# Kernel optimization log

Hardware: AMD Instinct MI355X
Metric: run time of the kernel (lower is better)

## Reference

```python
import jax, jax.numpy as jnp
import numpy as np
from jax import lax

B, T, S, J, D = 8, 512, 32, 64, 400
R, MDU, TAGS = 256, 100, 7


def _lstm(x, Wih, Whh, bih, bhh):
    """PyTorch-convention LSTM over x [N,L,Din]; gate order i,f,g,o.
    Returns (hs, cs) each [N,L,R] in scan order (not re-flipped)."""
    N = x.shape[0]
    Rh = Whh.shape[1]
    h0 = jnp.zeros((N, Rh), x.dtype)
    xW = x @ Wih.T + (bih + bhh)  # precompute input projection [N,L,4R]

    def step(carry, xt):
        h, c = carry
        g = xt + h @ Whh.T
        i, f, gg, o = jnp.split(g, 4, axis=-1)
        c = jax.nn.sigmoid(f) * c + jax.nn.sigmoid(i) * jnp.tanh(gg)
        h = jax.nn.sigmoid(o) * jnp.tanh(c)
        return (h, c), (h, c)

    _, (hs, cs) = lax.scan(step, (h0, h0), xW.transpose(1, 0, 2))
    return hs.transpose(1, 0, 2), cs.transpose(1, 0, 2)


def setup_inputs() -> dict:
    key = jax.random.key(0)
    ks = jax.random.split(key, 40)

    def rn(i, shape, s=0.1):
        return s * jax.random.normal(ks[i], shape, jnp.float32)

    inp = {
        'input_text': rn(0, (B, T, D), 1.0),
        'input_syn': rn(1, (B, S, J, D), 1.0),
        'label': jax.random.randint(ks[2], (B, T), 0, TAGS),
        'len_context': jnp.full((B,), T, jnp.int32),
        'len_synopsis': jnp.full((B, S), J, jnp.int32),
    }
    # 6 LSTM parameter sets: context f1/b1 (in=D), synopsis f/b (in=D), modeling f/b (in=4R)
    idx = 3
    for name, din in [('f1', D), ('b1', D), ('sf', D), ('sb', D), ('mf', 4 * R), ('mb', 4 * R)]:
        inp['Wih_' + name] = rn(idx, (4 * R, din)); idx += 1
        inp['Whh_' + name] = rn(idx, (4 * R, R)); idx += 1
        inp['bih_' + name] = rn(idx, (4 * R,)); idx += 1
        inp['bhh_' + name] = rn(idx, (4 * R,)); idx += 1
    inp['W_cWh'] = rn(idx, (MDU, 2 * R)); idx += 1
    inp['W_cWu'] = rn(idx, (MDU, 2 * R)); idx += 1
    inp['W_v'] = rn(idx, (1, MDU)); idx += 1
    inp['W_sWh'] = rn(idx, (2 * R, 2 * R)); idx += 1
    inp['W_sWu'] = rn(idx, (2 * R, 2 * R)); idx += 1
    inp['W_Ws'] = rn(idx, (MDU, 2 * R)); idx += 1
    inp['W_out'] = rn(idx, (TAGS, 6 * R)); idx += 1
    inp['b_out'] = rn(idx, (TAGS,)); idx += 1
    return inp


def reference(input_text, input_syn, label, len_context, len_synopsis,
              Wih_f1, Whh_f1, bih_f1, bhh_f1,
              Wih_b1, Whh_b1, bih_b1, bhh_b1,
              Wih_sf, Whh_sf, bih_sf, bhh_sf,
              Wih_sb, Whh_sb, bih_sb, bhh_sb,
              Wih_mf, Whh_mf, bih_mf, bhh_mf,
              Wih_mb, Whh_mb, bih_mb, bhh_mb,
              W_cWh, W_cWu, W_v, W_sWh, W_sWu, W_Ws, W_out, b_out):
    B_, T_, D_ = input_text.shape
    S_, J_ = input_syn.shape[1], input_syn.shape[2]

    mask = (jnp.arange(T_)[None, :] < len_context[:, None]).astype(input_text.dtype)

    # --- representation layer: manual bi-LSTMCell; backward hiddens kept in scan order ---
    hs_f, cs_f = _lstm(input_text, Wih_f1, Whh_f1, bih_f1, bhh_f1)
    hs_b, cs_b = _lstm(input_text[:, ::-1], Wih_b1, Whh_b1, bih_b1, bhh_b1)
    H = jnp.concatenate([hs_f, hs_b], -1) * mask[..., None]   # [B,T,2R]
    m = jnp.concatenate([cs_f, cs_b], -1) * mask[..., None]   # [B,T,2R]
    x_init = jnp.zeros((B_, 1, 2 * R), input_text.dtype)
    H_full = jnp.concatenate([x_init, H], 1)                  # H_ : [B,T+1,2R]

    # --- synopsis encoder: bi-LSTM final hidden per synopsis sentence ---
    syn = input_syn.reshape(B_ * S_, J_, D_)
    sh_f, _ = _lstm(syn, Wih_sf, Whh_sf, bih_sf, bhh_sf)
    sh_b, _ = _lstm(syn[:, ::-1], Wih_sb, Whh_sb, bih_sb, bhh_sb)
    U = jnp.concatenate([sh_f[:, -1], sh_b[:, -1]], -1).reshape(B_, S_, 2 * R)

    # --- 'ff' co-attention ---
    cWh = H @ W_cWh.T                                          # [B,T,MDU]
    cWu = U @ W_cWu.T                                          # [B,S,MDU]
    z = jnp.tanh(cWh[:, :, None, :] + cWu[:, None, :, :]) @ W_v[0]  # [B,T,S]
    alpha = jax.nn.softmax(z, axis=-1)
    c = jnp.einsum('bts,bsd->btd', alpha, U)                   # [B,T,2R]

    # --- sentinel (ATT_SYN) ---
    Hprev = H_full[:, :T_]                                     # shifted: x_init, H[0..T-2]
    e = jax.nn.sigmoid(Hprev @ W_sWh.T + Hprev @ W_sWu.T)
    s = e * jnp.tanh(m)                                        # [B,T,2R]
    z_hat = jnp.tanh(s @ W_Ws.T + cWh) @ W_v[0]                # [B,T]
    alpha_hat = jax.nn.softmax(jnp.concatenate([z, z_hat[..., None]], -1), axis=-1)
    beta = alpha_hat[:, :, S_:S_ + 1]                          # [B,T,1]
    c_hat = beta * s + (1.0 - beta) * c
    G = jnp.concatenate([H, c_hat], -1)                        # [B,T,4R]

    # --- modeling bi-LSTM (standard aligned outputs) + output projection ---
    mh_f, _ = _lstm(G, Wih_mf, Whh_mf, bih_mf, bhh_mf)
    mh_b, _ = _lstm(G[:, ::-1], Wih_mb, Whh_mb, bih_mb, bhh_mb)
    M = jnp.concatenate([mh_f, mh_b[:, ::-1]], -1)             # [B,T,2R]

    logit = jnp.concatenate([G, M], -1) @ W_out.T + b_out      # [B,T,TAGS]
    return logit
```

## Files before the change

### kernel.cpp

```cpp
#include <hip/hip_runtime.h>
#include <math.h>
#include <stddef.h>


#define BB 8
#define TT 512
#define SS 32
#define JJ 64
#define DD 400
#define RR 256
#define G4 1024
#define H2 512
#define MDU_ 100
#define TAGS_ 7
#define BT (BB*TT)
#define NSEQ (BB*SS)
#define SCH 64
#define MB1 (1024*1024)

typedef __attribute__((ext_vector_type(8))) short short8;
typedef __attribute__((ext_vector_type(4))) float floatx4;
typedef __attribute__((ext_vector_type(4))) unsigned int u32x4;
typedef unsigned short u16;
typedef unsigned int u32;

struct Ptr6 { const void* p[6]; };

__device__ __forceinline__ float us2f(u16 u) {
    unsigned int v = ((unsigned int)u) << 16;
    return __builtin_bit_cast(float, v);
}
__device__ __forceinline__ u16 f2us(float f) {
    unsigned int v = __builtin_bit_cast(unsigned int, f);
    v += 0x7FFFu + ((v >> 16) & 1u);
    return (u16)(v >> 16);
}
__device__ __forceinline__ float ldin(const void* p, long i, int bf) {
    return bf ? us2f(((const u16*)p)[i]) : ((const float*)p)[i];
}
__device__ __forceinline__ float sigm_f(float x) { return 1.0f / (1.0f + __expf(-x)); }
__device__ __forceinline__ float tanh_f(float x) {
    float e = __expf(-2.0f * fabsf(x));
    float t = (1.0f - e) / (1.0f + e);
    return copysignf(t, x);
}

__global__ void detect_k(const void* x, int* flag) {
    __shared__ int cnt;
    if (threadIdx.x == 0) cnt = 0;
    __syncthreads();
    u16 lo = ((const u16*)x)[threadIdx.x * 2];
    int e = (lo >> 7) & 0xFF;
    if (e >= 118 && e <= 131) atomicAdd(&cnt, 1);
    __syncthreads();
    if (threadIdx.x == 0) *flag = (cnt > 128) ? 1 : 0;
}
__global__ void castbf_k(const void* src, long off, u16* dst, long n, const int* flag) {
    long i = (long)blockIdx.x * 256 + threadIdx.x;
    if (i < n) dst[i] = (*flag) ? ((const u16*)src)[off + i] : f2us(((const float*)src)[off + i]);
}

__global__ void prep_k(const int* __restrict__ flag,
    const void* Wcwh, const void* Wcwu, const void* Wws, const void* Wout,
    const void* Wv, const void* bout, const void* WsWh, const void* WsWu,
    u16* Wcwh16, u16* Wcwu16, u16* Wws16, u16* Wout16,
    float* WvF, float* boutF, u16* WsumB, float* bsumAll,
    Ptr6 bih, Ptr6 bhh, Ptr6 whh, u16* WFall, u32* cnts)
{
    const int bf = *flag;
    long i = (long)blockIdx.x * 256 + threadIdx.x;
    if (i < 51200) { Wcwh16[i] = f2us(ldin(Wcwh, i, bf)); return; }
    i -= 51200;
    if (i < 51200) { Wcwu16[i] = f2us(ldin(Wcwu, i, bf)); return; }
    i -= 51200;
    if (i < 51200) { Wws16[i] = f2us(ldin(Wws, i, bf)); return; }
    i -= 51200;
    if (i < 10752) { Wout16[i] = f2us(ldin(Wout, i, bf)); return; }
    i -= 10752;
    if (i < 100) { WvF[i] = ldin(Wv, i, bf); return; }
    i -= 100;
    if (i < 7) { boutF[i] = ldin(bout, i, bf); return; }
    i -= 7;
    if (i < 6 * 1024) {
        int l = (int)(i >> 10), k = (int)(i & 1023);
        bsumAll[l * 1024 + k] = ldin(bih.p[l], k, bf) + ldin(bhh.p[l], k, bf);
        return;
    }
    i -= 6 * 1024;
    if (i < 262144) { WsumB[i] = f2us(ldin(WsWh, i, bf) + ldin(WsWu, i, bf)); return; }
    i -= 262144;
    if (i < 6L * 262144) {
        int l  = (int)(i >> 18);
        int ii = (int)(i & 262143);
        int j  = ii & 7;
        int ln = (ii >> 3) & 63;
        int c  = (ii >> 9) & 7;
        int t  = (ii >> 12) & 3;
        int w  = (ii >> 14) & 3;
        int s  = (ii >> 16) & 3;
        int n_g = w * 256 + s * 64 + t * 16 + (ln & 15);
        int k   = c * 32 + (ln >> 4) * 8 + j;
        WFall[(size_t)l * 262144 + ii] = f2us(ldin(whh.p[l], (long)n_g * 256 + k, bf));
        return;
    }
    i -= 6L * 262144;
    if (i < 8192) cnts[i] = 0u;
}

__global__ void castAB_k(const void* xsyn, u16* mx16,
                         const void* wih2, u16* mW16a,
                         const void* wih3, u16* mW16b,
                         const void* xtext, u16* x16c,
                         const void* wih0, u16* W16ac,
                         const void* wih1, u16* W16bc,
                         const int* __restrict__ flag)
{
    const int bf = *flag;
    long i = (long)blockIdx.x * 256 + threadIdx.x;
    const long nsyn = (long)NSEQ * JJ * DD;
    const long nw   = (long)G4 * DD;
    const long ntxt = (long)BT * DD;
    if (i < nsyn) { mx16[i] = f2us(ldin(xsyn, i, bf)); return; }
    i -= nsyn;
    if (i < nw) { mW16a[i] = f2us(ldin(wih2, i, bf)); return; }
    i -= nw;
    if (i < nw) { mW16b[i] = f2us(ldin(wih3, i, bf)); return; }
    i -= nw;
    if (i < ntxt) { x16c[i] = f2us(ldin(xtext, i, bf)); return; }
    i -= ntxt;
    if (i < nw) { W16ac[i] = f2us(ldin(wih0, i, bf)); return; }
    i -= nw;
    if (i < nw) { W16bc[i] = f2us(ldin(wih1, i, bf)); return; }
}

__global__ void cast3_k(const void* s0, u16* d0, long n0,
                        const void* s1, u16* d1, long n1,
                        const void* s2, u16* d2, long n2,
                        const int* __restrict__ flag)
{
    const int bf = *flag;
    long i = (long)blockIdx.x * 256 + threadIdx.x;
    if (i < n0) { d0[i] = f2us(ldin(s0, i, bf)); return; }
    i -= n0;
    if (i < n1) { d1[i] = f2us(ldin(s1, i, bf)); return; }
    i -= n1;
    if (i < n2) { d2[i] = f2us(ldin(s2, i, bf)); return; }
}

#define BM 128
#define BN 128
#define BK 32
#define LDT 40

__global__ __launch_bounds__(256)
void gemm_bt(const u16* __restrict__ A, int lda,
             const u16* __restrict__ W, int ldw,
             void* __restrict__ C, int ldc,
             const float* __restrict__ bias,
             int M, int N, int K, int outBf16)
{
    __shared__ alignas(16) short As[BM * LDT];
    __shared__ alignas(16) short Bs[BN * LDT];
    const int tid  = threadIdx.x;
    const int m0   = blockIdx.y * BM;
    const int n0   = blockIdx.x * BN;
    const int lane = tid & 63;
    const int wave = tid >> 6;
    const int wm   = wave >> 1, wn = wave & 1;
    const int quad = lane >> 4, mrow = lane & 15;

    floatx4 acc[4][4];
#pragma unroll
    for (int i = 0; i < 4; ++i)
#pragma unroll
        for (int j = 0; j < 4; ++j) { floatx4 z4 = {0.f,0.f,0.f,0.f}; acc[i][j] = z4; }

    for (int k0 = 0; k0 < K; k0 += BK) {
#pragma unroll
        for (int cc = 0; cc < 2; ++cc) {
            int c   = tid + cc * 256;
            int row = c >> 2;
            int kc  = (c & 3) << 3;
            int gk  = k0 + kc;
            {
                int gr = m0 + row;
                short8 v;
                if (gr < M && gk + 8 <= K) {
                    v = *(const short8*)(A + (size_t)gr * lda + gk);
                } else {
#pragma unroll
                    for (int e = 0; e < 8; ++e)
                        v[e] = (gr < M && (gk + e) < K) ? (short)A[(size_t)gr * lda + gk + e] : (short)0;
                }
                *(short8*)&As[row * LDT + kc] = v;
            }
            {
                int gn = n0 + row;
                short8 v;
                if (gn < N && gk + 8 <= K) {
                    v = *(const short8*)(W + (size_t)gn * ldw + gk);
                } else {
#pragma unroll
                    for (int e = 0; e < 8; ++e)
                        v[e] = (gn < N && (gk + e) < K) ? (short)W[(size_t)gn * ldw + gk + e] : (short)0;
                }
                *(short8*)&Bs[row * LDT + kc] = v;
            }
        }
        __syncthreads();

        short8 af[4], bf[4];
#pragma unroll
        for (int i = 0; i < 4; ++i)
            af[i] = *(const short8*)&As[(wm * 64 + i * 16 + mrow) * LDT + quad * 8];
#pragma unroll
        for (int j = 0; j < 4; ++j)
            bf[j] = *(const short8*)&Bs[(wn * 64 + j * 16 + mrow) * LDT + quad * 8];
#pragma unroll
        for (int i = 0; i < 4; ++i)
#pragma unroll
            for (int j = 0; j < 4; ++j)
                acc[i][j] = __builtin_amdgcn_mfma_f32_16x16x32_bf16(af[i], bf[j], acc[i][j], 0, 0, 0);
        __syncthreads();
    }

#pragma unroll
    for (int i = 0; i < 4; ++i)
#pragma unroll
        for (int j = 0; j < 4; ++j)
#pragma unroll
            for (int r = 0; r < 4; ++r) {
                int row = m0 + wm * 64 + i * 16 + quad * 4 + r;
                int col = n0 + wn * 64 + j * 16 + mrow;
                if (row < M && col < N) {
                    float v = acc[i][j][r];
                    if (bias) v += bias[col];
                    if (outBf16) ((u16*)C)[(size_t)row * ldc + col] = f2us(v);
                    else         ((float*)C)[(size_t)row * ldc + col] = v;
                }
            }
}

__global__ __launch_bounds__(256, 1)
void lstm_coop(const u16* __restrict__ xWf, const u16* __restrict__ xWb,
               const u16* __restrict__ WFf, const u16* __restrict__ WFb,
               int L,
               u16* __restrict__ hOut, int hStride,
               u16* __restrict__ cOut, int cStride,
               const int* __restrict__ lenp,
               int writeAtSource, int lastOnly, int seqBase,
               u32* __restrict__ hx32, u32* __restrict__ flags,
               int grpBase, int nb, int G8)
{
    const int wgid = blockIdx.x;
    const int s    = wgid / G8;
    const int g    = wgid - s * G8;
    if (g >= 2 * nb) return;
    const int dir  = g / nb;
    const int bat  = g - dir * nb;
    const int tid = threadIdx.x;
    const int wv  = tid >> 6;
    const int ln  = tid & 63;
    const int q   = ln >> 4, m = ln & 15;
    const u16* xW = dir ? xWb : xWf;
    const u16* WF = dir ? WFb : WFf;
    const int grp = grpBase + g;
    u32* flg = flags + (size_t)grp * 64;
    u32* hx  = hx32 + (size_t)grp * 2048;

    __shared__ float g_s[4 * 8 * 64];

    short8 bw[4][8];
    {
        const u16* wb = WF + ((size_t)(s * 4 + wv) * 32) * 512 + ln * 8;
#pragma unroll
        for (int t4 = 0; t4 < 4; ++t4)
#pragma unroll
            for (int c = 0; c < 8; ++c)
                bw[t4][c] = *(const short8*)(wb + (size_t)(t4 * 8 + c) * 512);
    }

    const int seqU = tid >> 5;
    const int j0   = (tid & 31) * 2;
    const int gcol = s * 64 + j0;
    const int mylen = lenp ? lenp[bat * 8 + seqU] : 0x7fffffff;
    float cR0 = 0.f, cR1 = 0.f;

    u32 px0, px1, px2, px3;
    {
        const int tt0 = dir ? (L - 1) : 0;
        const u16* xr = xW + (((size_t)(bat * 8 + seqU)) * L + tt0) * G4 + gcol;
        px0 = *(const u32*)xr;
        px1 = *(const u32*)(xr + 256);
        px2 = *(const u32*)(xr + 512);
        px3 = *(const u32*)(xr + 768);
    }

    for (int t = 0; t < L; ++t) {
        const int tt = dir ? (L - 1 - t) : t;
        short8 a[8];
        if (t > 0) {
            const u32* hp = hx + ((t - 1) & 1) * 1024 + m * 128;
#pragma unroll
            for (int c = 0; c < 8; ++c) {
                if (m < 8) {
                    u32x4 v = *(const u32x4*)(hp + c * 16 + q * 4);
                    a[c] = __builtin_bit_cast(short8, v);
                } else {
                    short8 z = {0,0,0,0,0,0,0,0}; a[c] = z;
                }
            }
        } else {
            short8 z = {0,0,0,0,0,0,0,0};
#pragma unroll
            for (int c = 0; c < 8; ++c) a[c] = z;
        }
        floatx4 acc[4];
#pragma unroll
        for (int t4 = 0; t4 < 4; ++t4) { floatx4 z4 = {0.f,0.f,0.f,0.f}; acc[t4] = z4; }
#pragma unroll
        for (int c = 0; c < 8; ++c)
#pragma unroll
            for (int t4 = 0; t4 < 4; ++t4)
                acc[t4] = __builtin_amdgcn_mfma_f32_16x16x32_bf16(a[c], bw[t4][c], acc[t4], 0, 0, 0);
        if (q < 2) {
#pragma unroll
            for (int t4 = 0; t4 < 4; ++t4)
#pragma unroll
                for (int r = 0; r < 4; ++r)
                    g_s[(wv * 8 + q * 4 + r) * 64 + t4 * 16 + m] = acc[t4][r];
        }
        __syncthreads();
        float hn0, hn1, cn0, cn1;
        {
            float i0 = g_s[(0 * 8 + seqU) * 64 + j0]     + us2f((u16)(px0 & 0xffffu));
            float i1 = g_s[(0 * 8 + seqU) * 64 + j0 + 1] + us2f((u16)(px0 >> 16));
            float f0 = g_s[(1 * 8 + seqU) * 64 + j0]     + us2f((u16)(px1 & 0xffffu));
            float f1 = g_s[(1 * 8 + seqU) * 64 + j0 + 1] + us2f((u16)(px1 >> 16));
            float g0 = g_s[(2 * 8 + seqU) * 64 + j0]     + us2f((u16)(px2 & 0xffffu));
            float g1 = g_s[(2 * 8 + seqU) * 64 + j0 + 1] + us2f((u16)(px2 >> 16));
            float o0 = g_s[(3 * 8 + seqU) * 64 + j0]     + us2f((u16)(px3 & 0xffffu));
            float o1 = g_s[(3 * 8 + seqU) * 64 + j0 + 1] + us2f((u16)(px3 >> 16));
            cn0 = sigm_f(f0) * cR0 + sigm_f(i0) * tanh_f(g0);
            cn1 = sigm_f(f1) * cR1 + sigm_f(i1) * tanh_f(g1);
            hn0 = sigm_f(o0) * tanh_f(cn0);
            hn1 = sigm_f(o1) * tanh_f(cn1);
            cR0 = cn0;
            cR1 = cn1;
            u32 hpack = (u32)f2us(hn0) | ((u32)f2us(hn1) << 16);
            __hip_atomic_store(hx + (t & 1) * 1024 + seqU * 128 + (gcol >> 1),
                               hpack, __ATOMIC_RELAXED, __HIP_MEMORY_SCOPE_AGENT);
        }
        asm volatile("s_waitcnt vmcnt(0)" ::: "memory");
        __syncthreads();
        const bool last = (t == L - 1);
        if (tid == 0 && !last)
            __hip_atomic_store(&flg[s * 16], (u32)(t + 1),
                               __ATOMIC_RELEASE, __HIP_MEMORY_SCOPE_AGENT);
        if (!lastOnly) {
            int wr = writeAtSource ? tt : t;
            float mk = (wr >= mylen) ? 0.f : 1.f;
            size_t ro = ((size_t)(bat * 8 + seqU)) * L + wr;
            u32 hp2 = (u32)f2us(hn0 * mk) | ((u32)f2us(hn1 * mk) << 16);
            *(u32*)(hOut + ro * hStride + dir * RR + gcol) = hp2;
            if (cOut) {
                u32 cp2 = (u32)f2us(cn0 * mk) | ((u32)f2us(cn1 * mk) << 16);
                *(u32*)(cOut + ro * cStride + dir * RR + gcol) = cp2;
            }
        } else if (last) {
            size_t ro = (size_t)(seqBase + bat * 8 + seqU);
            u32 hp2 = (u32)f2us(hn0) | ((u32)f2us(hn1) << 16);
            *(u32*)(hOut + ro * hStride + dir * RR + gcol) = hp2;
        }
        if (!last) {
            {
                const int tn = dir ? (L - 2 - t) : (t + 1);
                const u16* xr = xW + (((size_t)(bat * 8 + seqU)) * L + tn) * G4 + gcol;
                px0 = *(const u32*)xr;
                px1 = *(const u32*)(xr + 256);
                px2 = *(const u32*)(xr + 512);
                px3 = *(const u32*)(xr + 768);
            }
            if (tid == 0) {
                const u32 tgt = (u32)(t + 1);
                long guard = 0;
                for (;;) {
                    u32 f0 = __hip_atomic_load(&flg[0],  __ATOMIC_RELAXED, __HIP_MEMORY_SCOPE_AGENT);
                    u32 f1 = __hip_atomic_load(&flg[16], __ATOMIC_RELAXED, __HIP_MEMORY_SCOPE_AGENT);
                    u32 f2 = __hip_atomic_load(&flg[32], __ATOMIC_RELAXED, __HIP_MEMORY_SCOPE_AGENT);
                    u32 f3 = __hip_atomic_load(&flg[48], __ATOMIC_RELAXED, __HIP_MEMORY_SCOPE_AGENT);
                    if (f0 >= tgt && f1 >= tgt && f2 >= tgt && f3 >= tgt) break;
                    if (++guard > (1L << 18)) break;
                    if (guard > 32) __builtin_amdgcn_s_sleep(1);
                }
                __builtin_amdgcn_fence(__ATOMIC_ACQUIRE, "agent");
            }
            __syncthreads();
        }
    }
}

__global__ void hprev_k(const u16* __restrict__ G, u16* __restrict__ Hp) {
    int idx = blockIdx.x * 256 + threadIdx.x;
    if (idx < BT * H2) {
        int r = idx >> 9, d = idx & 511;
        int t = r & (TT - 1);
        Hp[idx] = (t == 0) ? (u16)0 : G[(size_t)(r - 1) * G4 + d];
    }
}
__global__ void s_k(const float* __restrict__ e, const u16* __restrict__ mB,
                    u16* __restrict__ sB) {
    int i = blockIdx.x * 256 + threadIdx.x;
    if (i < BT * H2) sB[i] = f2us(sigm_f(e[i]) * tanh_f(us2f(mB[i])));
}
__global__ void z_k(const float* __restrict__ cWh, const float* __restrict__ cWu,
                    const float* __restrict__ Wv, float* __restrict__ z) {
    int idx = blockIdx.x * 256 + threadIdx.x;
    if (idx >= BT * SS) return;
    int r = idx >> 5, s = idx & 31;
    int b = r >> 9;
    const float* ph = cWh + (size_t)r * MDU_;
    const float* pu = cWu + (size_t)(b * SS + s) * MDU_;
    float acc = 0.f;
#pragma unroll 4
    for (int j = 0; j < MDU_; ++j) acc += tanh_f(ph[j] + pu[j]) * Wv[j];
    z[idx] = acc;
}
__global__ void zhat_k(const float* __restrict__ sW, const float* __restrict__ cWh,
                       const float* __restrict__ Wv, float* __restrict__ zhat) {
    int r = blockIdx.x * 256 + threadIdx.x;
    if (r >= BT) return;
    float acc = 0.f;
    const float* ps = sW + (size_t)r * MDU_;
    const float* ph = cWh + (size_t)r * MDU_;
#pragma unroll 4
    for (int j = 0; j < MDU_; ++j) acc += tanh_f(ps[j] + ph[j]) * Wv[j];
    zhat[r] = acc;
}
__global__ __launch_bounds__(64)
void attn_mix_k(const float* __restrict__ z, const float* __restrict__ zhat,
                const u16* __restrict__ U, const u16* __restrict__ sB,
                u16* __restrict__ G) {
    int r = blockIdx.x;
    int lane = threadIdx.x;
    int b = r >> 9;
    __shared__ float alpha[SS];
    float zv = (lane < SS) ? z[(size_t)r * SS + lane] : -1e30f;
    float mx = zv;
    for (int o = 32; o > 0; o >>= 1) mx = fmaxf(mx, __shfl_xor(mx, o));
    float ez = (lane < SS) ? expf(zv - mx) : 0.f;
    float s1 = ez;
    for (int o = 32; o > 0; o >>= 1) s1 += __shfl_xor(s1, o);
    float zh = zhat[r];
    float mx2 = fmaxf(mx, zh);
    float denom = s1 * expf(mx - mx2) + expf(zh - mx2);
    float beta = expf(zh - mx2) / denom;
    if (lane < SS) alpha[lane] = ez / s1;
    __syncthreads();
    for (int d = lane; d < H2; d += 64) {
        float cv = 0.f;
#pragma unroll 8
        for (int s2 = 0; s2 < SS; ++s2)
            cv += alpha[s2] * us2f(U[(size_t)(b * SS + s2) * H2 + d]);
        float sv = us2f(sB[(size_t)r * H2 + d]);
        G[(size_t)r * G4 + H2 + d] = f2us(beta * sv + (1.f - beta) * cv);
    }
}
__global__ __launch_bounds__(256)
void logit_k(const u16* __restrict__ G, const u16* __restrict__ Mb,
             const u16* __restrict__ Wout, const float* __restrict__ boutF,
             void* __restrict__ out, const int* __restrict__ flag) {
    int r = blockIdx.x * 4 + (threadIdx.x >> 6);
    if (r >= BT) return;
    int lane = threadIdx.x & 63;
    float acc[TAGS_] = {0, 0, 0, 0, 0, 0, 0};
    for (int k = lane; k < 1536; k += 64) {
        float v = (k < G4) ? us2f(G[(size_t)r * G4 + k]) : us2f(Mb[(size_t)r * H2 + (k - G4)]);
#pragma unroll
        for (int tg = 0; tg < TAGS_; ++tg) acc[tg] += v * us2f(Wout[tg * 1536 + k]);
    }
#pragma unroll
    for (int tg = 0; tg < TAGS_; ++tg) {
        float s = acc[tg];
        for (int o = 32; o > 0; o >>= 1) s += __shfl_xor(s, o);
        acc[tg] = s;
    }
    if (lane == 0) {
        int bf = *flag;
#pragma unroll
        for (int tg = 0; tg < TAGS_; ++tg) {
            float v = acc[tg] + boutF[tg];
            if (bf) ((u16*)out)[(size_t)r * TAGS_ + tg] = f2us(v);
            else    ((float*)out)[(size_t)r * TAGS_ + tg] = v;
        }
    }
}

extern "C" void kernel_launch(void* const* d_in, const int* in_sizes, int n_in,
                              void* d_out, int out_size, void* d_ws, size_t ws_size,
                              hipStream_t stream)
{
    const void* x_text = d_in[0];
    const void* x_syn  = d_in[1];
    const int* len_ctx = (const int*)d_in[3];
    const void *Wih[6], *Whh[6], *bih[6], *bhh[6];
    for (int l = 0; l < 6; ++l) {
        Wih[l] = d_in[5 + l * 4 + 0];
        Whh[l] = d_in[5 + l * 4 + 1];
        bih[l] = d_in[5 + l * 4 + 2];
        bhh[l] = d_in[5 + l * 4 + 3];
    }
    const void* W_cWh = d_in[29];
    const void* W_cWu = d_in[30];
    const void* W_v   = d_in[31];
    const void* W_sWh = d_in[32];
    const void* W_sWu = d_in[33];
    const void* W_Ws  = d_in[34];
    const void* W_out = d_in[35];
    const void* b_out = d_in[36];
    (void)in_sizes; (void)n_in; (void)out_size;

    char* ws = (char*)d_ws;
    size_t off = 0;
    auto alloc = [&](size_t bytes) -> void* {
        void* p = ws + off;
        off += (bytes + 255) & ~(size_t)255;
        return p;
    };
    int*   flagB  = (int*)alloc(256);
    float* bsumAll = (float*)alloc((size_t)6 * G4 * 4);
    u16*   WsumB  = (u16*)alloc((size_t)H2 * H2 * 2);
    u16*   Ub     = (u16*)alloc((size_t)NSEQ * H2 * 2);
    u16*   Gb     = (u16*)alloc((size_t)BT * G4 * 2);
    u16*   mMb    = (u16*)alloc((size_t)BT * H2 * 2);
    float* cWhB   = (float*)alloc((size_t)BT * MDU_ * 4);
    float* cWuB   = (float*)alloc((size_t)NSEQ * MDU_ * 4);
    float* sWB    = (float*)alloc((size_t)BT * MDU_ * 4);
    float* zB     = (float*)alloc((size_t)BT * SS * 4);
    float* zhatB  = (float*)alloc((size_t)BT * 4);
    u16*   Wcwh16 = (u16*)alloc((size_t)MDU_ * H2 * 2);
    u16*   Wcwu16 = (u16*)alloc((size_t)MDU_ * H2 * 2);
    u16*   Wws16  = (u16*)alloc((size_t)MDU_ * H2 * 2);
    u16*   Wout16 = (u16*)alloc((size_t)TAGS_ * 1536 * 2);
    float* WvF    = (float*)alloc((size_t)MDU_ * 4);
    float* boutF  = (float*)alloc((size_t)TAGS_ * 4);
    u16*   WFall  = (u16*)alloc((size_t)6 * G4 * RR * 2);
    u16*   WF[6];
    for (int l = 0; l < 6; ++l) WF[l] = WFall + (size_t)l * G4 * RR;
    float* bsum[6];
    for (int l = 0; l < 6; ++l) bsum[l] = bsumAll + (size_t)l * G4;
    u32*   cnts   = (u32*)alloc((size_t)128 * 64 * 4);
    u32*   hx32   = (u32*)alloc((size_t)128 * 2048 * 4);

    size_t fixedEnd = off;
    bool bigws = (ws_size >= fixedEnd + (size_t)81 * MB1);
    char* BIG = (char*)alloc(bigws ? (size_t)80 * MB1 : (size_t)24 * MB1);

    u16*   bufA  = (u16*)BIG;
    u16*   bufB  = (u16*)(BIG + (size_t)8 * MB1);
    u16*   x16   = (u16*)(BIG + (size_t)16 * MB1);
    u16*   W16a  = (u16*)(BIG + (size_t)19 * MB1 + MB1 / 2);
    u16*   W16b  = (u16*)(BIG + (size_t)20 * MB1 + MB1 / 2);
    u16*   HprevB = (u16*)BIG;
    float* eBuf   = (float*)(BIG + (size_t)4 * MB1);
    u16*   sBuf   = (u16*)(BIG + (size_t)12 * MB1);
    u16*   mxWf  = (u16*)BIG;
    u16*   mxWb  = (u16*)(BIG + (size_t)8 * MB1);
    u16*   W16aD = (u16*)(BIG + (size_t)16 * MB1);
    u16*   W16bD = (u16*)(BIG + (size_t)18 * MB1);
    u16*   mbufA = (u16*)BIG;
    u16*   mbufB = (u16*)(BIG + (size_t)32 * MB1);
    u16*   mx16  = (u16*)(BIG + (size_t)64 * MB1);
    u16*   mW16a = (u16*)(BIG + (size_t)78 * MB1);
    u16*   mW16b = (u16*)(BIG + (size_t)79 * MB1);
    u16*   bufAc = (u16*)(BIG + (size_t)64 * MB1);
    u16*   bufBc = (u16*)(BIG + (size_t)72 * MB1);
    u16*   x16c  = Gb;
    u16*   W16ac = mMb;
    u16*   W16bc = mMb + (size_t)G4 * DD;

    auto cgrid = [](long n) { return dim3((unsigned)((n + 255) / 256)); };

    Ptr6 pBih, pBhh, pWhh;
    for (int l = 0; l < 6; ++l) { pBih.p[l] = bih[l]; pBhh.p[l] = bhh[l]; pWhh.p[l] = Whh[l]; }

    detect_k<<<dim3(1), dim3(256), 0, stream>>>(x_text, flagB);
    {
        long nprep = 51200L * 3 + 10752 + 100 + 7 + 6 * 1024 + 262144 + 6L * 262144 + 8192;
        prep_k<<<cgrid(nprep), dim3(256), 0, stream>>>(
            flagB, W_cWh, W_cWu, W_Ws, W_out, W_v, b_out, W_sWh, W_sWu,
            Wcwh16, Wcwu16, Wws16, Wout16, WvF, boutF, WsumB, bsumAll,
            pBih, pBhh, pWhh, WFall, cnts);
    }

    if (bigws) {
        {
            long ncast = (long)NSEQ * JJ * DD + 4L * G4 * DD + (long)BT * DD;
            castAB_k<<<cgrid(ncast), dim3(256), 0, stream>>>(
                x_syn, mx16, Wih[2], mW16a, Wih[3], mW16b,
                x_text, x16c, Wih[0], W16ac, Wih[1], W16bc, flagB);
        }
        gemm_bt<<<dim3(8, (NSEQ * JJ) / BM), dim3(256), 0, stream>>>(mx16, DD, mW16a, DD, mbufA, G4, bsum[2], NSEQ * JJ, G4, DD, 1);
        gemm_bt<<<dim3(8, (NSEQ * JJ) / BM), dim3(256), 0, stream>>>(mx16, DD, mW16b, DD, mbufB, G4, bsum[3], NSEQ * JJ, G4, DD, 1);
        gemm_bt<<<dim3(8, 32), dim3(256), 0, stream>>>(x16c, DD, W16ac, DD, bufAc, G4, bsum[0], BT, G4, DD, 1);
        gemm_bt<<<dim3(8, 32), dim3(256), 0, stream>>>(x16c, DD, W16bc, DD, bufBc, G4, bsum[1], BT, G4, DD, 1);
        lstm_coop<<<dim3(256), dim3(256), 0, stream>>>(
            mbufA, mbufB, WF[2], WF[3], JJ,
            Ub, H2, (u16*)nullptr, 0, (const int*)nullptr,
            0, 1, 0, hx32, cnts, 4, 32, 64);
        lstm_coop<<<dim3(32), dim3(256), 0, stream>>>(
            bufAc, bufBc, WF[0], WF[1], TT,
            Gb, G4, mMb, H2, len_ctx, 0, 0, 0, hx32, cnts, 0, 1, 8);
    } else {
        castbf_k<<<cgrid(G4 * DD), dim3(256), 0, stream>>>(Wih[2], 0, W16a, G4 * DD, flagB);
        castbf_k<<<cgrid(G4 * DD), dim3(256), 0, stream>>>(Wih[3], 0, W16b, G4 * DD, flagB);
        for (int c = 0; c < NSEQ / SCH; ++c) {
            long chunkElems = (long)SCH * JJ * DD;
            castbf_k<<<cgrid(chunkElems), dim3(256), 0, stream>>>(x_syn, (long)c * chunkElems, x16, chunkElems, flagB);
            gemm_bt<<<dim3(8, (SCH * JJ) / BM), dim3(256), 0, stream>>>(x16, DD, W16a, DD, bufA, G4, bsum[2], SCH * JJ, G4, DD, 1);
            gemm_bt<<<dim3(8, (SCH * JJ) / BM), dim3(256), 0, stream>>>(x16, DD, W16b, DD, bufB, G4, bsum[3], SCH * JJ, G4, DD, 1);
            lstm_coop<<<dim3(64), dim3(256), 0, stream>>>(
                bufA, bufB, WF[2], WF[3], JJ,
                Ub, H2, (u16*)nullptr, 0, (const int*)nullptr,
                0, 1, c * SCH, hx32, cnts, 4 + c * 16, 8, 16);
        }
        castbf_k<<<cgrid((long)BT * DD), dim3(256), 0, stream>>>(x_text, 0, x16, (long)BT * DD, flagB);
        castbf_k<<<cgrid(G4 * DD), dim3(256), 0, stream>>>(Wih[0], 0, W16a, G4 * DD, flagB);
        castbf_k<<<cgrid(G4 * DD), dim3(256), 0, stream>>>(Wih[1], 0, W16b, G4 * DD, flagB);
        gemm_bt<<<dim3(8, 32), dim3(256), 0, stream>>>(x16, DD, W16a, DD, bufA, G4, bsum[0], BT, G4, DD, 1);
        gemm_bt<<<dim3(8, 32), dim3(256), 0, stream>>>(x16, DD, W16b, DD, bufB, G4, bsum[1], BT, G4, DD, 1);
        lstm_coop<<<dim3(32), dim3(256), 0, stream>>>(
            bufA, bufB, WF[0], WF[1], TT,
            Gb, G4, mMb, H2, len_ctx, 0, 0, 0, hx32, cnts, 0, 1, 8);
    }

    gemm_bt<<<dim3(1, 32), dim3(256), 0, stream>>>(Gb, G4, Wcwh16, H2, cWhB, MDU_, nullptr, BT, MDU_, H2, 0);
    gemm_bt<<<dim3(1, 2),  dim3(256), 0, stream>>>(Ub, H2, Wcwu16, H2, cWuB, MDU_, nullptr, NSEQ, MDU_, H2, 0);
    hprev_k<<<cgrid(BT * H2), dim3(256), 0, stream>>>(Gb, HprevB);
    gemm_bt<<<dim3(4, 32), dim3(256), 0, stream>>>(HprevB, H2, WsumB, H2, eBuf, H2, nullptr, BT, H2, H2, 0);
    s_k<<<cgrid(BT * H2), dim3(256), 0, stream>>>(eBuf, mMb, sBuf);
    gemm_bt<<<dim3(1, 32), dim3(256), 0, stream>>>(sBuf, H2, Wws16, H2, sWB, MDU_, nullptr, BT, MDU_, H2, 0);
    z_k<<<cgrid(BT * SS), dim3(256), 0, stream>>>(cWhB, cWuB, WvF, zB);
    zhat_k<<<cgrid(BT), dim3(256), 0, stream>>>(sWB, cWhB, WvF, zhatB);
    attn_mix_k<<<dim3(BT), dim3(64), 0, stream>>>(zB, zhatB, Ub, sBuf, Gb);

    cast3_k<<<cgrid(2L * G4 * G4), dim3(256), 0, stream>>>(
        Wih[4], W16aD, (long)G4 * G4, Wih[5], W16bD, (long)G4 * G4,
        nullptr, nullptr, 0, flagB);
    gemm_bt<<<dim3(8, 32), dim3(256), 0, stream>>>(Gb, G4, W16aD, G4, mxWf, G4, bsum[4], BT, G4, G4, 1);
    gemm_bt<<<dim3(8, 32), dim3(256), 0, stream>>>(Gb, G4, W16bD, G4, mxWb, G4, bsum[5], BT, G4, G4, 1);
    lstm_coop<<<dim3(32), dim3(256), 0, stream>>>(
        mxWf, mxWb, WF[4], WF[5], TT,
        mMb, H2, (u16*)nullptr, 0, (const int*)nullptr, 1, 0, 0, hx32, cnts, 2, 1, 8);

    logit_k<<<dim3(BT / 4), dim3(256), 0, stream>>>(Gb, mMb, Wout16, boutF, d_out, flagB);
}
```

Measured before the change: 4.023 ms.

## Replace flag barrier in LSTM recurrence with timestep-tagged hidden-state polling

Hidden-state exchange between cooperating workgroups now packs the timestep tag into the upper half of each 64-bit word, and readers spin until every word they need carries the expected tag. This removes the separate release-flag store, the single-thread flag poll, the vmcnt wait and one workgroup barrier per step. The cost is doubled exchange buffer size, heavier polling traffic from many lanes, and an extra zeroing pass in the prep kernel.

Result: slower. 4.498 ms (+11.8%).

```diff
diff --git a/kernel.cpp b/kernel.cpp
--- a/kernel.cpp
+++ b/kernel.cpp
@@ -23,6 +23,7 @@
 typedef __attribute__((ext_vector_type(4))) unsigned int u32x4;
 typedef unsigned short u16;
 typedef unsigned int u32;
+typedef unsigned long long u64;
 
 struct Ptr6 { const void* p[6]; };
 
@@ -65,7 +66,7 @@
     const void* Wv, const void* bout, const void* WsWh, const void* WsWu,
     u16* Wcwh16, u16* Wcwu16, u16* Wws16, u16* Wout16,
     float* WvF, float* boutF, u16* WsumB, float* bsumAll,
-    Ptr6 bih, Ptr6 bhh, Ptr6 whh, u16* WFall, u32* cnts)
+    Ptr6 bih, Ptr6 bhh, Ptr6 whh, u16* WFall, u32* cnts, u32* hxz)
 {
     const int bf = *flag;
     long i = (long)blockIdx.x * 256 + threadIdx.x;
@@ -104,7 +105,9 @@
         return;
     }
     i -= 6L * 262144;
-    if (i < 8192) cnts[i] = 0u;
+    if (i < 8192) { cnts[i] = 0u; return; }
+    i -= 8192;
+    if (i < 1048576) hxz[i] = 0u;
 }
 
 __global__ void castAB_k(const void* xsyn, u16* mx16,
@@ -249,7 +252,7 @@
                u16* __restrict__ cOut, int cStride,
                const int* __restrict__ lenp,
                int writeAtSource, int lastOnly, int seqBase,
-               u32* __restrict__ hx32, u32* __restrict__ flags,
+               u64* __restrict__ hx64, u32* __restrict__ flags,
                int grpBase, int nb, int G8)
 {
     const int wgid = blockIdx.x;
@@ -265,8 +268,8 @@
     const u16* xW = dir ? xWb : xWf;
     const u16* WF = dir ? WFb : WFf;
     const int grp = grpBase + g;
-    u32* flg = flags + (size_t)grp * 64;
-    u32* hx  = hx32 + (size_t)grp * 2048;
+    (void)flags;
+    u64* hx = hx64 + (size_t)grp * 2048;
 
     __shared__ float g_s[4 * 8 * 64];
 
@@ -299,16 +302,33 @@
     for (int t = 0; t < L; ++t) {
         const int tt = dir ? (L - 1 - t) : t;
         short8 a[8];
-        if (t > 0) {
-            const u32* hp = hx + ((t - 1) & 1) * 1024 + m * 128;
+        if (t > 0 && m < 8) {
+            const u64* hp = hx + ((t - 1) & 1) * 1024 + m * 128 + q * 4;
+            const u32 want = (u32)t;
+            u64 v[8][4];
+            long guard = 0;
+            for (;;) {
+#pragma unroll
+                for (int c = 0; c < 8; ++c)
+#pragma unroll
+                    for (int e = 0; e < 4; ++e)
+                        v[c][e] = __hip_atomic_load(hp + c * 16 + e,
+                                                    __ATOMIC_RELAXED,
+                                                    __HIP_MEMORY_SCOPE_AGENT);
+                bool ok = true;
+#pragma unroll
+                for (int c = 0; c < 8; ++c)
+#pragma unroll
+                    for (int e = 0; e < 4; ++e)
+                        ok &= ((u32)(v[c][e] >> 32) == want);
+                if (ok) break;
+                if (++guard > (1L << 18)) break;
+                if (guard > 64) __builtin_amdgcn_s_sleep(1);
+            }
 #pragma unroll
             for (int c = 0; c < 8; ++c) {
-                if (m < 8) {
-                    u32x4 v = *(const u32x4*)(hp + c * 16 + q * 4);
-                    a[c] = __builtin_bit_cast(short8, v);
-                } else {
-                    short8 z = {0,0,0,0,0,0,0,0}; a[c] = z;
-                }
+                u32x4 d = { (u32)v[c][0], (u32)v[c][1], (u32)v[c][2], (u32)v[c][3] };
+                a[c] = __builtin_bit_cast(short8, d);
             }
         } else {
             short8 z = {0,0,0,0,0,0,0,0};
@@ -348,15 +368,11 @@
             cR0 = cn0;
             cR1 = cn1;
             u32 hpack = (u32)f2us(hn0) | ((u32)f2us(hn1) << 16);
+            u64 pk = ((u64)(u32)(t + 1) << 32) | (u64)hpack;
             __hip_atomic_store(hx + (t & 1) * 1024 + seqU * 128 + (gcol >> 1),
-                               hpack, __ATOMIC_RELAXED, __HIP_MEMORY_SCOPE_AGENT);
-        }
-        asm volatile("s_waitcnt vmcnt(0)" ::: "memory");
-        __syncthreads();
+                               pk, __ATOMIC_RELAXED, __HIP_MEMORY_SCOPE_AGENT);
+        }
         const bool last = (t == L - 1);
-        if (tid == 0 && !last)
-            __hip_atomic_store(&flg[s * 16], (u32)(t + 1),
-                               __ATOMIC_RELEASE, __HIP_MEMORY_SCOPE_AGENT);
         if (!lastOnly) {
             int wr = writeAtSource ? tt : t;
             float mk = (wr >= mylen) ? 0.f : 1.f;
@@ -373,30 +389,14 @@
             *(u32*)(hOut + ro * hStride + dir * RR + gcol) = hp2;
         }
         if (!last) {
-            {
-                const int tn = dir ? (L - 2 - t) : (t + 1);
-                const u16* xr = xW + (((size_t)(bat * 8 + seqU)) * L + tn) * G4 + gcol;
-                px0 = *(const u32*)xr;
-                px1 = *(const u32*)(xr + 256);
-                px2 = *(const u32*)(xr + 512);
-                px3 = *(const u32*)(xr + 768);
-            }
-            if (tid == 0) {
-                const u32 tgt = (u32)(t + 1);
-                long guard = 0;
-                for (;;) {
-                    u32 f0 = __hip_atomic_load(&flg[0],  __ATOMIC_RELAXED, __HIP_MEMORY_SCOPE_AGENT);
-                    u32 f1 = __hip_atomic_load(&flg[16], __ATOMIC_RELAXED, __HIP_MEMORY_SCOPE_AGENT);
-                    u32 f2 = __hip_atomic_load(&flg[32], __ATOMIC_RELAXED, __HIP_MEMORY_SCOPE_AGENT);
-                    u32 f3 = __hip_atomic_load(&flg[48], __ATOMIC_RELAXED, __HIP_MEMORY_SCOPE_AGENT);
-                    if (f0 >= tgt && f1 >= tgt && f2 >= tgt && f3 >= tgt) break;
-                    if (++guard > (1L << 18)) break;
-                    if (guard > 32) __builtin_amdgcn_s_sleep(1);
-                }
-                __builtin_amdgcn_fence(__ATOMIC_ACQUIRE, "agent");
-            }
-            __syncthreads();
-        }
+            const int tn = dir ? (L - 2 - t) : (t + 1);
+            const u16* xr = xW + (((size_t)(bat * 8 + seqU)) * L + tn) * G4 + gcol;
+            px0 = *(const u32*)xr;
+            px1 = *(const u32*)(xr + 256);
+            px2 = *(const u32*)(xr + 512);
+            px3 = *(const u32*)(xr + 768);
+        }
+        __syncthreads();
     }
 }
 
@@ -550,7 +550,7 @@
     float* bsum[6];
     for (int l = 0; l < 6; ++l) bsum[l] = bsumAll + (size_t)l * G4;
     u32*   cnts   = (u32*)alloc((size_t)128 * 64 * 4);
-    u32*   hx32   = (u32*)alloc((size_t)128 * 2048 * 4);
+    u64*   hx64   = (u64*)alloc((size_t)128 * 2048 * 8);
 
     size_t fixedEnd = off;
     bool bigws = (ws_size >= fixedEnd + (size_t)81 * MB1);
@@ -586,11 +586,12 @@
 
     detect_k<<<dim3(1), dim3(256), 0, stream>>>(x_text, flagB);
     {
-        long nprep = 51200L * 3 + 10752 + 100 + 7 + 6 * 1024 + 262144 + 6L * 262144 + 8192;
+        long nprep = 51200L * 3 + 10752 + 100 + 7 + 6 * 1024 + 262144
+                   + 6L * 262144 + 8192 + 1048576;
         prep_k<<<cgrid(nprep), dim3(256), 0, stream>>>(
             flagB, W_cWh, W_cWu, W_Ws, W_out, W_v, b_out, W_sWh, W_sWu,
             Wcwh16, Wcwu16, Wws16, Wout16, WvF, boutF, WsumB, bsumAll,
-            pBih, pBhh, pWhh, WFall, cnts);
+            pBih, pBhh, pWhh, WFall, cnts, (u32*)hx64);
     }
 
     if (bigws) {
@@ -607,10 +608,10 @@
         lstm_coop<<<dim3(256), dim3(256), 0, stream>>>(
             mbufA, mbufB, WF[2], WF[3], JJ,
             Ub, H2, (u16*)nullptr, 0, (const int*)nullptr,
-            0, 1, 0, hx32, cnts, 4, 32, 64);
+            0, 1, 0, hx64, cnts, 4, 32, 64);
         lstm_coop<<<dim3(32), dim3(256), 0, stream>>>(
             bufAc, bufBc, WF[0], WF[1], TT,
-            Gb, G4, mMb, H2, len_ctx, 0, 0, 0, hx32, cnts, 0, 1, 8);
+            Gb, G4, mMb, H2, len_ctx, 0, 0, 0, hx64, cnts, 0, 1, 8);
     } else {
         castbf_k<<<cgrid(G4 * DD), dim3(256), 0, stream>>>(Wih[2], 0, W16a, G4 * DD, flagB);
         castbf_k<<<cgrid(G4 * DD), dim3(256), 0, stream>>>(Wih[3], 0, W16b, G4 * DD, flagB);
@@ -622,7 +623,7 @@
             lstm_coop<<<dim3(64), dim3(256), 0, stream>>>(
                 bufA, bufB, WF[2], WF[3], JJ,
                 Ub, H2, (u16*)nullptr, 0, (const int*)nullptr,
-                0, 1, c * SCH, hx32, cnts, 4 + c * 16, 8, 16);
+                0, 1, c * SCH, hx64, cnts, 4 + c * 16, 8, 16);
         }
         castbf_k<<<cgrid((long)BT * DD), dim3(256), 0, stream>>>(x_text, 0, x16, (long)BT * DD, flagB);
         castbf_k<<<cgrid(G4 * DD), dim3(256), 0, stream>>>(Wih[0], 0, W16a, G4 * DD, flagB);
@@ -631,7 +632,7 @@
         gemm_bt<<<dim3(8, 32), dim3(256), 0, stream>>>(x16, DD, W16b, DD, bufB, G4, bsum[1], BT, G4, DD, 1);
         lstm_coop<<<dim3(32), dim3(256), 0, stream>>>(
             bufA, bufB, WF[0], WF[1], TT,
-            Gb, G4, mMb, H2, len_ctx, 0, 0, 0, hx32, cnts, 0, 1, 8);
+            Gb, G4, mMb, H2, len_ctx, 0, 0, 0, hx64, cnts, 0, 1, 8);
     }
 
     gemm_bt<<<dim3(1, 32), dim3(256), 0, stream>>>(Gb, G4, Wcwh16, H2, cWhB, MDU_, nullptr, BT, MDU_, H2, 0);
@@ -651,7 +652,7 @@
     gemm_bt<<<dim3(8, 32), dim3(256), 0, stream>>>(Gb, G4, W16bD, G4, mxWb, G4, bsum[5], BT, G4, G4, 1);
     lstm_coop<<<dim3(32), dim3(256), 0, stream>>>(
         mxWf, mxWb, WF[4], WF[5], TT,
-        mMb, H2, (u16*)nullptr, 0, (const int*)nullptr, 1, 0, 0, hx32, cnts, 2, 1, 8);
+        mMb, H2, (u16*)nullptr, 0, (const int*)nullptr, 1, 0, 0, hx64, cnts, 2, 1, 8);
 
     logit_k<<<dim3(BT / 4), dim3(256), 0, stream>>>(Gb, mMb, Wout16, boutF, d_out, flagB);
 }
```
